# Performance work log

Hardware: AMD Instinct MI355X
Metric: run time of the kernel (lower is better)

Reference implementation:

```python
import jax, jax.numpy as jnp
import numpy as np

B, N, C, H = 2, 1024, 768, 12
D = C // H
SCALE = D ** -0.5


def setup_inputs() -> dict:
    key = jax.random.key(0)
    ks = jax.random.split(key, 6)
    s = 1.0 / np.sqrt(C)
    return {
        "x": jax.random.normal(ks[0], (B, N, C), jnp.float32),
        "Wqkv": jax.random.normal(ks[1], (3 * C, C), jnp.float32) * s,   # qkv_bias=False
        "Wa": jax.random.normal(ks[2], (H, C), jnp.float32) * s,        # selective gate Linear(dim, H)
        "ba": jnp.zeros((H,), jnp.float32),
        "Wproj": jax.random.normal(ks[3], (C, C), jnp.float32) * s,
        "bproj": jnp.zeros((C,), jnp.float32),
    }


def _silu_shifted(z):
    # silu(x) + 0.5, L2-normalized over head dim (silunorm=True)
    r = jax.nn.silu(z) + 0.5
    return r / jnp.linalg.norm(r, axis=-1, keepdims=True)


def _forward(x, Wqkv, Wa, ba, Wproj, bproj):
    qkv = (x @ Wqkv.T).reshape(B, N, 3, H, D).transpose(2, 0, 3, 1, 4)  # [3,B,H,N,D]
    q = _silu_shifted(qkv[0])
    k = _silu_shifted(qkv[1])
    v = qkv[2]

    # selective forget gates: a = 1 - sigmoid(Linear(x)); torch.tensor(...) detaches -> stop_gradient
    a = jax.lax.stop_gradient(1.0 - jax.nn.sigmoid(x @ Wa.T + ba)).transpose(0, 2, 1)  # [B,H,N]
    # drop first token's gate, prepend 1 (as in the module)
    a = jnp.concatenate([jnp.ones_like(a[..., :1]), a[..., 1:]], axis=-1)

    # Causal_Mask_Selective(log(a)):
    #   A_for[i,j]  = prod_{t=j..i-1} a[t]   (j <= i)
    #   A_back[i,j] = prod_{t=i+1..j} a[t]   (j >= i)
    #   M = A_for + A_back - I
    c = jnp.cumsum(jnp.log(a), axis=-1)
    c = jnp.concatenate([jnp.zeros_like(c[..., :1]), c], axis=-1)  # [B,H,N+1], c[m] = sum log a[0..m-1]
    tri = jnp.tril(jnp.ones((N, N), bool))
    d_for = c[..., :N, None] - c[..., None, :N]      # c[i]-c[j]
    d_back = c[..., None, 1:] - c[..., 1:, None]     # c[j+1]-c[i+1]
    A_for = jnp.where(tri, jnp.exp(jnp.where(tri, d_for, 0.0)), 0.0)
    A_back = jnp.where(tri.T, jnp.exp(jnp.where(tri.T, d_back, 0.0)), 0.0)
    M = A_for + A_back - jnp.eye(N, dtype=x.dtype)

    attn = jnp.einsum('bhid,bhjd->bhij', q, k) * SCALE * M
    attn = attn / (attn.sum(axis=-1, keepdims=True) + 1e-6)  # sum-normalization, NOT softmax
    out = jnp.einsum('bhij,bhjd->bhid', attn, v).transpose(0, 2, 1, 3).reshape(B, N, C)
    return out @ Wproj.T + bproj


def reference(x, Wqkv, Wa, ba, Wproj, bproj):
    return _forward(x, Wqkv, Wa, ba, Wproj, bproj)
```

## Files before the change

kernel.cpp:

```cpp
#include <hip/hip_runtime.h>
#include <hip/hip_bf16.h>

#define BB 2
#define NN 1024
#define CC 768
#define HH 12
#define DD 64
#define SCALE_F 0.125f

typedef __attribute__((ext_vector_type(8))) __bf16 bf16x8;
typedef __attribute__((ext_vector_type(8))) unsigned short u16x8;
typedef __attribute__((ext_vector_type(4))) unsigned short u16x4;
typedef __attribute__((ext_vector_type(4))) float f32x4;

static __device__ __forceinline__ bf16x8 as_bf16x8(u16x8 v) {
  return __builtin_bit_cast(bf16x8, v);
}
static __device__ __forceinline__ unsigned short bf16u(float f) {
  __hip_bfloat16 h = __float2bfloat16(f);
  return __builtin_bit_cast(unsigned short, h);
}
static __device__ __forceinline__ void gload16(const void* g, void* l) {
  __builtin_amdgcn_global_load_lds(
      (const __attribute__((address_space(1))) unsigned int*)g,
      (__attribute__((address_space(3))) unsigned int*)l, 16, 0, 0);
}

__global__ __launch_bounds__(256) void packgate(
    const float* __restrict__ x, const float* __restrict__ Wa,
    const float* __restrict__ ba, float* __restrict__ loga,
    unsigned short* __restrict__ xb, int n0,
    const float* __restrict__ Wqkv, unsigned short* __restrict__ wqkvb, int n1,
    const float* __restrict__ Wproj, unsigned short* __restrict__ wprojb,
    int n2) {
  __shared__ float was[HH][CC];
  if (blockIdx.x < 512) {
    for (int i = threadIdx.x; i < HH * CC; i += 256)
      was[i / CC][i % CC] = Wa[i];
    __syncthreads();
    const int w = threadIdx.x >> 6, lane = threadIdx.x & 63;
    const int row = blockIdx.x * 4 + w;
    const int b = row >> 10, n = row & 1023;
    const float* xr = x + (size_t)row * CC;
    float xf[12];
#pragma unroll
    for (int j = 0; j < 12; j++) xf[j] = xr[lane + 64 * j];
    float myacc = 0.f;
#pragma unroll
    for (int h = 0; h < HH; h++) {
      float a = 0.f;
#pragma unroll
      for (int j = 0; j < 12; j++) a += xf[j] * was[h][lane + 64 * j];
#pragma unroll
      for (int off = 32; off >= 1; off >>= 1) a += __shfl_xor(a, off, 64);
      if (lane == h) myacc = a;
    }
    if (lane < HH) {
      float acc = myacc + ba[lane];
      float a = 1.f - 1.f / (1.f + __expf(-acc));
      float la = (n == 0) ? 0.f : log2f(a);
      loga[(b * HH + lane) * NN + n] = la;
    }
  } else {
    int i = (blockIdx.x - 512) * 256 + threadIdx.x;
    const float* s;
    unsigned short* d;
    if (i < n0) {
      s = x; d = xb;
    } else if (i < n0 + n1) {
      i -= n0; s = Wqkv; d = wqkvb;
    } else {
      i -= n0 + n1;
      if (i >= n2) return;
      s = Wproj; d = wprojb;
    }
    float4 v = ((const float4*)s)[i];
    u16x4 u = {bf16u(v.x), bf16u(v.y), bf16u(v.z), bf16u(v.w)};
    *(u16x4*)&d[i * 4] = u;
  }
}

template <int BM, int BN, int EPI>
__global__ __launch_bounds__(256) void gemm_mfma(
    const unsigned short* __restrict__ A, const unsigned short* __restrict__ W,
    const float* __restrict__ bias, void* __restrict__ outv,
    unsigned short* __restrict__ qp, unsigned short* __restrict__ kp,
    unsigned short* __restrict__ vtp, int M, int Nc, int K) {
  __shared__ unsigned short As[2][BM * 64];
  __shared__ unsigned short Ws[2][BN * 64];
  constexpr int FM = BM / 32, FN = BN / 32;
  const int row0 = blockIdx.y * BM;
  const int col0 = blockIdx.x * BN;
  const int t = threadIdx.x;
  const int w = t >> 6, lane = t & 63;
  const int lrow = lane & 15, lgrp = lane >> 4;
  const int wr = w >> 1, wc = w & 1;

  f32x4 acc[FM][FN] = {};

  auto STAGE = [&](int buf, int k0) {
#pragma unroll
    for (int i = 0; i < BM * 8 / 256; i++) {
      int idx = i * 256 + t;
      int row = idx >> 3, sl = (idx & 7) ^ (row & 7);
      gload16(A + (size_t)(row0 + row) * K + k0 + sl * 8, &As[buf][idx * 8]);
    }
#pragma unroll
    for (int i = 0; i < BN * 8 / 256; i++) {
      int idx = i * 256 + t;
      int row = idx >> 3, sl = (idx & 7) ^ (row & 7);
      gload16(W + (size_t)(col0 + row) * K + k0 + sl * 8, &Ws[buf][idx * 8]);
    }
  };

  const int NT = K / 64;
  STAGE(0, 0);
  __syncthreads();

  for (int tt = 0; tt < NT; tt++) {
    const int cur = tt & 1;
    if (tt + 1 < NT) STAGE(cur ^ 1, (tt + 1) * 64);

    bf16x8 af[FM][2], bf[FN][2];
#pragma unroll
    for (int m = 0; m < FM; m++) {
      int row = wr * (BM / 2) + m * 16 + lrow;
      const u16x8* p = (const u16x8*)&As[cur][row * 64];
#pragma unroll
      for (int hk = 0; hk < 2; hk++)
        af[m][hk] = as_bf16x8(p[(hk * 4 + lgrp) ^ (row & 7)]);
    }
#pragma unroll
    for (int n = 0; n < FN; n++) {
      int row = wc * (BN / 2) + n * 16 + lrow;
      const u16x8* p = (const u16x8*)&Ws[cur][row * 64];
#pragma unroll
      for (int hk = 0; hk < 2; hk++)
        bf[n][hk] = as_bf16x8(p[(hk * 4 + lgrp) ^ (row & 7)]);
    }
#pragma unroll
    for (int m = 0; m < FM; m++)
#pragma unroll
      for (int n = 0; n < FN; n++) {
        acc[m][n] = __builtin_amdgcn_mfma_f32_16x16x32_bf16(
            af[m][0], bf[n][0], acc[m][n], 0, 0, 0);
        acc[m][n] = __builtin_amdgcn_mfma_f32_16x16x32_bf16(
            af[m][1], bf[n][1], acc[m][n], 0, 0, 0);
      }
    __syncthreads();
  }

  if constexpr (EPI == 0) {
#pragma unroll
    for (int n = 0; n < FN; n++) {
      int col = col0 + wc * (BN / 2) + n * 16 + lrow;
      float bb = bias ? bias[col] : 0.f;
#pragma unroll
      for (int m = 0; m < FM; m++) {
        int rbase = row0 + wr * (BM / 2) + m * 16 + lgrp * 4;
#pragma unroll
        for (int r = 0; r < 4; r++)
          ((float*)outv)[(size_t)(rbase + r) * Nc + col] = acc[m][n][r] + bb;
      }
    }
  } else {
    const int sec = col0 / CC;
    const int h = ((col0 % CC) >> 6) + wc;
    const int rb = row0 + wr * (BM / 2);
    const int b = rb >> 10;
    const int nbase = rb & (NN - 1);
    const size_t bh = (size_t)b * HH + h;
    if (sec < 2) {
      unsigned short* dst = sec ? kp : qp;
#pragma unroll
      for (int m = 0; m < FM; m++) {
#pragma unroll
        for (int r = 0; r < 4; r++) {
          float sil[FN];
          float ss = 0.f;
#pragma unroll
          for (int n = 0; n < FN; n++) {
            float v = acc[m][n][r];
            float s = v / (1.f + __expf(-v)) + 0.5f;
            sil[n] = s;
            ss += s * s;
          }
#pragma unroll
          for (int off = 1; off <= 8; off <<= 1) ss += __shfl_xor(ss, off, 64);
          float rn = rsqrtf(ss);
          int nn = nbase + m * 16 + lgrp * 4 + r;
#pragma unroll
          for (int n = 0; n < FN; n++)
            dst[(bh * NN + nn) * DD + n * 16 + lrow] = bf16u(sil[n] * rn);
        }
      }
    } else {
#pragma unroll
      for (int m = 0; m < FM; m++) {
#pragma unroll
        for (int n = 0; n < FN; n++) {
          int d = n * 16 + lrow;
          int nn0 = nbase + m * 16 + lgrp * 4;
          u16x4 pkt = {bf16u(acc[m][n][0]), bf16u(acc[m][n][1]),
                       bf16u(acc[m][n][2]), bf16u(acc[m][n][3])};
          *(u16x4*)&vtp[(bh * DD + d) * NN + nn0] = pkt;
        }
      }
    }
  }
}

__global__ __launch_bounds__(256) void attn_mfma(
    const unsigned short* __restrict__ qp, const unsigned short* __restrict__ kp,
    const unsigned short* __restrict__ vt, const float* __restrict__ loga,
    unsigned short* __restrict__ attnout) {
  __shared__ __align__(16) unsigned char smem[45072];
  unsigned short* Ks = (unsigned short*)smem;
  unsigned short* Vs = (unsigned short*)(smem + 16384);
  unsigned short* AwB = (unsigned short*)(smem + 32768);
  float* cls = (float*)(smem + 40960);
  float* CwB = (float*)smem;
  float* RwB = (float*)(smem + 8704);

  const int qt2 = blockIdx.x & 31;
  const int bh = blockIdx.x >> 5;
  const int b = bh / HH, h = bh % HH;
  const int qrow0 = qt2 * 32;
  const int w = threadIdx.x >> 6;
  const int lane = threadIdx.x & 63;
  const int lrow = lane & 15;
  const int lgrp = lane >> 4;
  const int wq = w & 1;
  const int js = w >> 1;

  if (w == 0) {
    const float4* s4 = (const float4*)(loga + (size_t)bh * NN + lane * 16);
    float v[16];
#pragma unroll
    for (int q = 0; q < 4; q++) {
      float4 tv = s4[q];
      v[q * 4 + 0] = tv.x; v[q * 4 + 1] = tv.y;
      v[q * 4 + 2] = tv.z; v[q * 4 + 3] = tv.w;
    }
    float run = 0.f;
#pragma unroll
    for (int e = 0; e < 16; e++) { run += v[e]; v[e] = run; }
    float tot = run;
#pragma unroll
    for (int off = 1; off < 64; off <<= 1) {
      float nb = __shfl_up(tot, off, 64);
      if (lane >= off) tot += nb;
    }
    float excl = tot - run;
    if (lane == 0) cls[0] = 0.f;
#pragma unroll
    for (int e = 0; e < 16; e++) cls[1 + lane * 16 + e] = v[e] + excl;
  }

  bf16x8 qaf[2];
  {
    const u16x8* qrow_p = (const u16x8*)(qp +
        ((size_t)bh * NN + qrow0 + wq * 16 + lrow) * DD);
#pragma unroll
    for (int hk = 0; hk < 2; hk++) qaf[hk] = as_bf16x8(qrow_p[hk * 4 + lgrp]);
  }

  const int ibase = qrow0 + wq * 16 + lgrp * 4;
  float ci[4], ci1[4];
  f32x4 oacc[4] = {};
  float rs[4] = {0.f, 0.f, 0.f, 0.f};

  for (int t = 0; t < 8; t++) {
#pragma unroll
    for (int rep = 0; rep < 4; rep++) {
      int idx = rep * 256 + threadIdx.x;
      int buf = idx >> 9, row = (idx >> 3) & 63;
      int sl = (idx & 7) ^ (row & 7);
      int j0s = (buf * 8 + t) * 64;
      gload16(kp + ((size_t)bh * NN + j0s + row) * DD + sl * 8, Ks + idx * 8);
      gload16(vt + ((size_t)bh * DD + row) * NN + j0s + sl * 8, Vs + idx * 8);
    }
    __syncthreads();
    if (t == 0) {
#pragma unroll
      for (int r = 0; r < 4; r++) {
        ci[r] = cls[ibase + r];
        ci1[r] = cls[ibase + r + 1];
      }
    }

    const int j0 = (js * 8 + t) * 64;

#pragma unroll
    for (int ct = 0; ct < 4; ct++) {
      const int jl = ct * 16 + lrow;
      const int j = j0 + jl;
      f32x4 s = {};
      const u16x8* krow_p = (const u16x8*)(Ks + js * 4096 + jl * 64);
#pragma unroll
      for (int hk = 0; hk < 2; hk++) {
        bf16x8 kf = as_bf16x8(krow_p[(hk * 4 + lgrp) ^ (jl & 7)]);
        s = __builtin_amdgcn_mfma_f32_16x16x32_bf16(qaf[hk], kf, s, 0, 0, 0);
      }
      const float cj = cls[j], cj1 = cls[j + 1];
#pragma unroll
      for (int r = 0; r < 4; r++) {
        const int gi = ibase + r;
        float m = (gi > j) ? exp2f(ci[r] - cj)
                 : (gi < j) ? exp2f(cj1 - ci1[r]) : 1.0f;
        float av = s[r] * SCALE_F * m;
        rs[r] += av;
        int rowa = lgrp * 4 + r;
        AwB[w * 1024 + rowa * 64 + (jl ^ ((rowa & 7) << 3))] = bf16u(av);
      }
    }

#pragma unroll
    for (int jh = 0; jh < 2; jh++) {
      const u16x8* arow_p = (const u16x8*)(AwB + w * 1024 + lrow * 64);
      bf16x8 af = as_bf16x8(arow_p[(jh * 4 + lgrp) ^ (lrow & 7)]);
#pragma unroll
      for (int dt = 0; dt < 4; dt++) {
        const int dd = dt * 16 + lrow;
        const u16x8* vrow_p = (const u16x8*)(Vs + js * 4096 + dd * 64);
        bf16x8 vf = as_bf16x8(vrow_p[(jh * 4 + lgrp) ^ (dd & 7)]);
        oacc[dt] =
            __builtin_amdgcn_mfma_f32_16x16x32_bf16(af, vf, oacc[dt], 0, 0, 0);
      }
    }
    __syncthreads();
  }

#pragma unroll
  for (int r = 0; r < 4; r++) {
#pragma unroll
    for (int off = 1; off <= 8; off <<= 1) rs[r] += __shfl_xor(rs[r], off, 64);
  }

  if (w >= 2) {
#pragma unroll
    for (int dt = 0; dt < 4; dt++)
#pragma unroll
      for (int r = 0; r < 4; r++)
        CwB[((w - 2) * 64 + lane) * 17 + dt * 4 + r] = oacc[dt][r];
#pragma unroll
    for (int r = 0; r < 4; r++) RwB[((w - 2) * 64 + lane) * 5 + r] = rs[r];
  }
  __syncthreads();
  if (w < 2) {
#pragma unroll
    for (int r = 0; r < 4; r++) {
      rs[r] += RwB[(w * 64 + lane) * 5 + r];
      rs[r] = 1.f / (rs[r] + 1e-6f);
    }
#pragma unroll
    for (int dt = 0; dt < 4; dt++) {
#pragma unroll
      for (int r = 0; r < 4; r++) {
        const int gi = ibase + r;
        float val =
            (oacc[dt][r] + CwB[(w * 64 + lane) * 17 + dt * 4 + r]) * rs[r];
        attnout[((size_t)b * NN + gi) * CC + h * DD + dt * 16 + lrow] =
            bf16u(val);
      }
    }
  }
}

extern "C" void kernel_launch(void* const* d_in, const int* in_sizes, int n_in,
                              void* d_out, int out_size, void* d_ws,
                              size_t ws_size, hipStream_t stream) {
  const float* x = (const float*)d_in[0];
  const float* Wqkv = (const float*)d_in[1];
  const float* Wa = (const float*)d_in[2];
  const float* ba = (const float*)d_in[3];
  const float* Wproj = (const float*)d_in[4];
  const float* bproj = (const float*)d_in[5];
  float* out = (float*)d_out;

  unsigned short* obuf = (unsigned short*)d_ws;
  float* loga = (float*)(obuf + (size_t)BB * NN * CC);
  unsigned short* qp = (unsigned short*)(loga + (size_t)BB * HH * NN);
  unsigned short* kp = qp + (size_t)BB * HH * NN * DD;
  unsigned short* vt = kp + (size_t)BB * HH * NN * DD;
  unsigned short* xb = vt + (size_t)BB * HH * NN * DD;
  unsigned short* wqkvb = xb + (size_t)BB * NN * CC;
  unsigned short* wprojb = wqkvb + (size_t)3 * CC * CC;

  const int n0 = BB * NN * CC / 4, n1 = 3 * CC * CC / 4, n2 = CC * CC / 4;

  packgate<<<512 + (n0 + n1 + n2 + 255) / 256, 256, 0, stream>>>(
      x, Wa, ba, loga, xb, n0, Wqkv, wqkvb, n1, Wproj, wprojb, n2);
  {
    dim3 grid(3 * CC / 128, BB * NN / 64);
    gemm_mfma<64, 128, 2><<<grid, 256, 0, stream>>>(
        xb, wqkvb, nullptr, nullptr, qp, kp, vt, BB * NN, 3 * CC, CC);
  }
  attn_mfma<<<BB * HH * (NN / 32), 256, 0, stream>>>(qp, kp, vt, loga, obuf);
  {
    dim3 grid(CC / 64, BB * NN / 64);
    gemm_mfma<64, 64, 0><<<grid, 256, 0, stream>>>(
        obuf, wprojb, bproj, out, nullptr, nullptr, nullptr, BB * NN, CC, CC);
  }
}
```

Baseline: 128.7 us.

## Prefetch next K/V tile into registers during compute, add MFMA priority hints

Replaces the per-iteration direct global-to-LDS load followed by a barrier with a register prefetch. The loads for tile t+1 are issued before computing tile t, and the registers are written to swizzled LDS after the compute barrier, so global latency overlaps the MFMA work. It also wraps the MFMA sections in s_setprio to favour matrix-issuing waves. The cost is extra VGPRs for the staging registers and a second barrier per iteration, which may lower occupancy.

Result: no change. 130.7 us (+1.5%).

```diff
diff --git a/kernel.cpp b/kernel.cpp
--- a/kernel.cpp
+++ b/kernel.cpp
@@ -257,6 +257,16 @@
     for (int e = 0; e < 16; e++) cls[1 + lane * 16 + e] = v[e] + excl;
   }
 
+#pragma unroll
+  for (int rep = 0; rep < 4; rep++) {
+    int idx = rep * 256 + threadIdx.x;
+    int buf = idx >> 9, row = (idx >> 3) & 63;
+    int sl = (idx & 7) ^ (row & 7);
+    int j0s = buf * 8 * 64;
+    gload16(kp + ((size_t)bh * NN + j0s + row) * DD + sl * 8, Ks + idx * 8);
+    gload16(vt + ((size_t)bh * DD + row) * NN + j0s + sl * 8, Vs + idx * 8);
+  }
+
   bf16x8 qaf[2];
   {
     const u16x8* qrow_p = (const u16x8*)(qp +
@@ -266,26 +276,29 @@
   }
 
   const int ibase = qrow0 + wq * 16 + lgrp * 4;
-  float ci[4], ci1[4];
   f32x4 oacc[4] = {};
   float rs[4] = {0.f, 0.f, 0.f, 0.f};
 
+  __syncthreads();
+  float ci[4], ci1[4];
+#pragma unroll
+  for (int r = 0; r < 4; r++) {
+    ci[r] = cls[ibase + r];
+    ci1[r] = cls[ibase + r + 1];
+  }
+
+  u16x8 kreg[4], vreg[4];
   for (int t = 0; t < 8; t++) {
-#pragma unroll
-    for (int rep = 0; rep < 4; rep++) {
-      int idx = rep * 256 + threadIdx.x;
-      int buf = idx >> 9, row = (idx >> 3) & 63;
-      int sl = (idx & 7) ^ (row & 7);
-      int j0s = (buf * 8 + t) * 64;
-      gload16(kp + ((size_t)bh * NN + j0s + row) * DD + sl * 8, Ks + idx * 8);
-      gload16(vt + ((size_t)bh * DD + row) * NN + j0s + sl * 8, Vs + idx * 8);
-    }
-    __syncthreads();
-    if (t == 0) {
-#pragma unroll
-      for (int r = 0; r < 4; r++) {
-        ci[r] = cls[ibase + r];
-        ci1[r] = cls[ibase + r + 1];
+    if (t < 7) {
+#pragma unroll
+      for (int rep = 0; rep < 4; rep++) {
+        int idx = rep * 256 + threadIdx.x;
+        int buf = idx >> 9, row = (idx >> 3) & 63, slot = idx & 7;
+        int j0s = (buf * 8 + t + 1) * 64;
+        kreg[rep] =
+            *(const u16x8*)(kp + ((size_t)bh * NN + j0s + row) * DD + slot * 8);
+        vreg[rep] =
+            *(const u16x8*)(vt + ((size_t)bh * DD + row) * NN + j0s + slot * 8);
       }
     }
 
@@ -297,11 +310,13 @@
       const int j = j0 + jl;
       f32x4 s = {};
       const u16x8* krow_p = (const u16x8*)(Ks + js * 4096 + jl * 64);
+      __builtin_amdgcn_s_setprio(1);
 #pragma unroll
       for (int hk = 0; hk < 2; hk++) {
         bf16x8 kf = as_bf16x8(krow_p[(hk * 4 + lgrp) ^ (jl & 7)]);
         s = __builtin_amdgcn_mfma_f32_16x16x32_bf16(qaf[hk], kf, s, 0, 0, 0);
       }
+      __builtin_amdgcn_s_setprio(0);
       const float cj = cls[j], cj1 = cls[j + 1];
 #pragma unroll
       for (int r = 0; r < 4; r++) {
@@ -315,6 +330,7 @@
       }
     }
 
+    __builtin_amdgcn_s_setprio(1);
 #pragma unroll
     for (int jh = 0; jh < 2; jh++) {
       const u16x8* arow_p = (const u16x8*)(AwB + w * 1024 + lrow * 64);
@@ -328,7 +344,21 @@
             __builtin_amdgcn_mfma_f32_16x16x32_bf16(af, vf, oacc[dt], 0, 0, 0);
       }
     }
+    __builtin_amdgcn_s_setprio(0);
+
     __syncthreads();
+
+    if (t < 7) {
+#pragma unroll
+      for (int rep = 0; rep < 4; rep++) {
+        int idx = rep * 256 + threadIdx.x;
+        int buf = idx >> 9, row = (idx >> 3) & 63, slot = idx & 7;
+        int sw = slot ^ (row & 7);
+        *(u16x8*)(Ks + buf * 4096 + row * 64 + sw * 8) = kreg[rep];
+        *(u16x8*)(Vs + buf * 4096 + row * 64 + sw * 8) = vreg[rep];
+      }
+      __syncthreads();
+    }
   }
 
 #pragma unroll
```
